# Optimization experiments

Measured on AMD Instinct MI355X. Metric: run time of the kernel, lower is better.

Reference implementation:

```python
import jax, jax.numpy as jnp
import numpy as np
from jax import lax

B, T, I, H, L, C = 256, 512, 128, 256, 2, 10


def _lstm_layer(x_tm, lengths, W_ih, W_hh, b_ih, b_hh):
    # x_tm: [T, B, in]; lengths: [B]
    b = b_ih + b_hh  # [4H]
    h0 = jnp.zeros((x_tm.shape[1], H), x_tm.dtype)
    c0 = jnp.zeros_like(h0)

    def step(carry, inp):
        h, c = carry
        x_t, t = inp
        gates = x_t @ W_ih.T + h @ W_hh.T + b  # [B, 4H]
        i, f, g, o = jnp.split(gates, 4, axis=-1)
        i = jax.nn.sigmoid(i); f = jax.nn.sigmoid(f)
        g = jnp.tanh(g);        o = jax.nn.sigmoid(o)
        c_new = f * c + i * g
        h_new = o * jnp.tanh(c_new)
        m = (t < lengths)[:, None]  # freeze state past each sequence's length
        h = jnp.where(m, h_new, h)
        c = jnp.where(m, c_new, c)
        return (h, c), h

    (hT, cT), h_seq = lax.scan(step, (h0, c0), (x_tm, jnp.arange(x_tm.shape[0])))
    return h_seq, hT


def setup_inputs() -> dict:
    key = jax.random.key(0)
    ks = jax.random.split(key, 16)
    s_i = 1.0 / np.sqrt(H)
    inp = {
        'x': jax.random.normal(ks[0], (B, T, I), jnp.float32),
        'lengths': jax.random.randint(ks[1], (B,), 1, T + 1),
        'W_fc': jax.random.uniform(ks[2], (C, H), jnp.float32, -s_i, s_i),
        'b_fc': jax.random.uniform(ks[3], (C,), jnp.float32, -s_i, s_i),
    }
    for l in range(L):
        in_dim = I if l == 0 else H
        k0, k1, k2, k3 = jax.random.split(jax.random.fold_in(key, 100 + l), 4)
        inp[f'W_ih_{l}'] = jax.random.uniform(k0, (4 * H, in_dim), jnp.float32, -s_i, s_i)
        inp[f'W_hh_{l}'] = jax.random.uniform(k1, (4 * H, H), jnp.float32, -s_i, s_i)
        inp[f'b_ih_{l}'] = jax.random.uniform(k2, (4 * H,), jnp.float32, -s_i, s_i)
        inp[f'b_hh_{l}'] = jax.random.uniform(k3, (4 * H,), jnp.float32, -s_i, s_i)
    return inp


def reference(x, lengths, W_fc, b_fc,
              W_ih_0, W_hh_0, b_ih_0, b_hh_0,
              W_ih_1, W_hh_1, b_ih_1, b_hh_1):
    layer_params = [(W_ih_0, W_hh_0, b_ih_0, b_hh_0),
                    (W_ih_1, W_hh_1, b_ih_1, b_hh_1)]
    seq = jnp.swapaxes(x, 0, 1)  # [T, B, I] time-major
    hT = None
    for (W_ih, W_hh, b_ih, b_hh) in layer_params:
        seq, hT = _lstm_layer(seq, lengths, W_ih, W_hh, b_ih, b_hh)
    logits = hT @ W_fc.T + b_fc  # final hidden state of last layer
    return jax.nn.softmax(logits, axis=1)
```

## Files before the change

### kernel.cpp

```cpp
#include <hip/hip_runtime.h>

#define TT 512
#define BB 256
#define II 128
#define HH 256
#define CC 10

typedef __attribute__((ext_vector_type(8))) _Float16 f16x8;
typedef __attribute__((ext_vector_type(4))) _Float16 f16x4;
typedef __attribute__((ext_vector_type(4))) float    f32x4;

__device__ __forceinline__ float fsig(float x){ return 1.0f/(1.0f+__expf(-x)); }
__device__ __forceinline__ float ftanh(float x){ return 2.0f/(1.0f+__expf(-2.0f*x)) - 1.0f; }


template<bool FAST>
__device__ __forceinline__ unsigned cpoll(unsigned* p){
  unsigned v;
  if constexpr(FAST){
    unsigned z = 0u;
    asm volatile("global_atomic_add %0, %1, %2, off sc0\n\ts_waitcnt vmcnt(0)"
                 : "=v"(v) : "v"(p), "v"(z) : "memory");
  } else {
    v = __hip_atomic_fetch_add(p, 0u, __ATOMIC_RELAXED, __HIP_MEMORY_SCOPE_AGENT);
  }
  return v;
}
template<bool FAST>
__device__ __forceinline__ unsigned poll_until(unsigned* p, unsigned tgt){
  unsigned v = 0;
  if((threadIdx.x & 63) == 0){
    v = cpoll<FAST>(p);
    while(v < tgt){ __builtin_amdgcn_s_sleep(2); v = cpoll<FAST>(p); }
  }
  unsigned u = __builtin_amdgcn_readfirstlane(v);
  asm volatile("" ::: "memory");
  return u;
}
template<bool FAST>
__device__ __forceinline__ void arrive1(unsigned* p){
  if constexpr(FAST){
    unsigned one = 1u;
    asm volatile("global_atomic_add %0, %1, off" :: "v"(p), "v"(one) : "memory");
  } else {
    (void)__hip_atomic_fetch_add(p, 1u, __ATOMIC_RELAXED, __HIP_MEMORY_SCOPE_AGENT);
  }
}
template<bool FAST>
__device__ __forceinline__ void store_h16(_Float16* p, _Float16 vv){
  unsigned b32 = (unsigned)__builtin_bit_cast(unsigned short, vv);
  if constexpr(FAST)
    asm volatile("global_store_short %0, %1, off" :: "v"(p), "v"(b32) : "memory");
  else
    asm volatile("global_store_short %0, %1, off sc0 sc1" :: "v"(p), "v"(b32) : "memory");
}
template<bool FAST>
__device__ __forceinline__ f16x8 load_ring(const _Float16* p){
  f16x8 r;
  if constexpr(FAST)
    asm volatile("global_load_dwordx4 %0, %1, off sc0" : "=v"(r) : "v"(p) : "memory");
  else
    asm volatile("global_load_dwordx4 %0, %1, off sc0 sc1" : "=v"(r) : "v"(p) : "memory");
  return r;
}
#define PIN(x) asm volatile("" : "+v"(x))

template<int KXT, bool IS_L1, bool FAST>
__device__ __forceinline__ void run_wave(
    const _Float16* __restrict__ xin,
    const _Float16* __restrict__ Wh,
    const _Float16* __restrict__ Wx,
    const float* __restrict__ b_ih, const float* __restrict__ b_hh,
    const int* __restrict__ lengths,
    _Float16* __restrict__ hbuf,
    float* __restrict__ hT,
    unsigned* cown, unsigned* cprod, int gb, int gj)
{
  constexpr int KXV = KXT*32;
  const int lane = threadIdx.x & 63;
  const int quad = lane >> 4;
  const int l15  = lane & 15;
  const int koff = quad << 3;
  const int b0   = gb << 4;
  const int u    = (gj << 4) + l15;

  f16x8 wh[4][8], wx[4][KXT];
  float bias[4];
#pragma unroll
  for(int g=0; g<4; ++g){
    const int row = g*HH + u;
#pragma unroll
    for(int kt=0; kt<8; ++kt){
      wh[g][kt] = *(const f16x8*)(Wh + (size_t)row*HH + kt*32 + koff);
      PIN(wh[g][kt]);
    }
#pragma unroll
    for(int kt=0; kt<KXT; ++kt){
      wx[g][kt] = *(const f16x8*)(Wx + (size_t)row*KXV + kt*32 + koff);
      PIN(wx[g][kt]);
    }
    bias[g] = b_ih[row] + b_hh[row];
  }

  int sb[4], len[4]; float cs[4], hs[4];
#pragma unroll
  for(int r=0; r<4; ++r){
    sb[r]  = b0 + (quad<<2) + r;
    len[r] = lengths[sb[r]];
    cs[r] = 0.f; hs[r] = 0.f;
  }

  unsigned lastp = 0, lasto = 0;

  f16x8 axn[KXT];
  if(!IS_L1){
    const _Float16* xp = xin + ((size_t)(b0+l15)*TT + 0)*KXV + koff;
#pragma unroll
    for(int kt=0; kt<KXT; ++kt) axn[kt] = *(const f16x8*)(xp + kt*32);
  }

  for(int t=0; t<TT; ++t){
    f16x8 ax[KXT];
    if(IS_L1){
      const unsigned tgtp = 16u*(unsigned)(t+1);
      if(lastp < tgtp) lastp = poll_until<FAST>(cprod, tgtp);
      const _Float16* xp = xin + ((size_t)t*BB + b0 + l15)*HH + koff;
#pragma unroll
      for(int kt=0; kt<KXT; ++kt) ax[kt] = *(const f16x8*)(xp + kt*32);
    } else {
#pragma unroll
      for(int kt=0; kt<KXT; ++kt) ax[kt] = axn[kt];
    }

    if(t > 0){
      const unsigned tgto = 16u*(unsigned)t;
      if(lasto < tgto) lasto = poll_until<FAST>(cown, tgto);
    }
    f16x8 ah[8];
    if(t > 0){
      if(IS_L1){
        const _Float16* hp = hbuf + (((size_t)((t-1)&3))*BB + b0 + l15)*HH + koff;
#pragma unroll
        for(int kt=0; kt<8; ++kt) ah[kt] = load_ring<FAST>(hp + kt*32);
      } else {
        const _Float16* hp = hbuf + ((size_t)(t-1)*BB + b0 + l15)*HH + koff;
#pragma unroll
        for(int kt=0; kt<8; ++kt) ah[kt] = *(const f16x8*)(hp + kt*32);
      }
    }

    f32x4 acc[4];
#pragma unroll
    for(int g=0; g<4; ++g) acc[g] = (f32x4){bias[g],bias[g],bias[g],bias[g]};
#pragma unroll
    for(int kt=0; kt<KXT; ++kt)
#pragma unroll
      for(int g=0; g<4; ++g)
        acc[g] = __builtin_amdgcn_mfma_f32_16x16x32_f16(ax[kt], wx[g][kt], acc[g], 0,0,0);

    if(t > 0){
      if(IS_L1){
        asm volatile("s_waitcnt vmcnt(0)"
          : "+v"(ah[0]),"+v"(ah[1]),"+v"(ah[2]),"+v"(ah[3]),
            "+v"(ah[4]),"+v"(ah[5]),"+v"(ah[6]),"+v"(ah[7]) :: "memory");
      }
#pragma unroll
      for(int kt=0; kt<8; ++kt)
#pragma unroll
        for(int g=0; g<4; ++g)
          acc[g] = __builtin_amdgcn_mfma_f32_16x16x32_f16(ah[kt], wh[g][kt], acc[g], 0,0,0);
    }

#pragma unroll
    for(int r=0; r<4; ++r){
      float iv = fsig (acc[0][r]);
      float fv = fsig (acc[1][r]);
      float gv = ftanh(acc[2][r]);
      float ov = fsig (acc[3][r]);
      float cn = fv*cs[r] + iv*gv;
      float hn = ov*ftanh(cn);
      if(t < len[r]){ cs[r] = cn; hs[r] = hn; }
      _Float16* hp = IS_L1
        ? hbuf + (((size_t)(t&3))*BB + sb[r])*HH + u
        : hbuf + ((size_t)t*BB + sb[r])*HH + u;
      store_h16<FAST>(hp, (_Float16)hs[r]);
      if(IS_L1 && t == TT-1) hT[(size_t)sb[r]*HH + u] = hs[r];
    }

    asm volatile("s_waitcnt vmcnt(0)" ::: "memory");
    if(lane == 0) arrive1<FAST>(cown);

    if(!IS_L1 && t+1 < TT){
      const _Float16* xp = xin + ((size_t)(b0+l15)*TT + (t+1))*KXV + koff;
#pragma unroll
      for(int kt=0; kt<KXT; ++kt) axn[kt] = *(const f16x8*)(xp + kt*32);
    }
  }
}

__global__ __launch_bounds__(64, 1)
void lstm_fused(const _Float16* __restrict__ xc,
                const _Float16* __restrict__ Wh0, const _Float16* __restrict__ Wx0,
                const _Float16* __restrict__ Wh1, const _Float16* __restrict__ Wx1,
                const float* __restrict__ b_ih0, const float* __restrict__ b_hh0,
                const float* __restrict__ b_ih1, const float* __restrict__ b_hh1,
                const int* __restrict__ lens,
                _Float16* __restrict__ h0seq, _Float16* __restrict__ h1ring,
                float* __restrict__ hT, unsigned* __restrict__ ctr)
{
  const int blk   = blockIdx.x;
  const int layer = blk >> 8;
  const int gb    = blk & 15;
  const int gj    = (blk >> 4) & 15;
  const int lane  = threadIdx.x & 63;
  unsigned* c0    = ctr + gb*32;
  unsigned* c1    = ctr + (16+gb)*32;
  unsigned* xcds  = ctr + 1024;
  unsigned* cinit = ctr + 1536;

  unsigned myx;
  asm volatile("s_getreg_b32 %0, hwreg(HW_REG_XCC_ID)" : "=s"(myx));
  if(lane == 0){
    asm volatile("global_store_dword %0, %1, off sc0 sc1" :: "v"(xcds + blk), "v"(myx) : "memory");
    asm volatile("s_waitcnt vmcnt(0)" ::: "memory");
    (void)__hip_atomic_fetch_add(cinit, 1u, __ATOMIC_RELAXED, __HIP_MEMORY_SCOPE_AGENT);
  }
  unsigned iv = 0;
  if(lane == 0){
    iv = __hip_atomic_fetch_add(cinit, 0u, __ATOMIC_RELAXED, __HIP_MEMORY_SCOPE_AGENT);
    while(iv < 512u){ __builtin_amdgcn_s_sleep(8);
      iv = __hip_atomic_fetch_add(cinit, 0u, __ATOMIC_RELAXED, __HIP_MEMORY_SCOPE_AGENT); }
  }
  (void)__builtin_amdgcn_readfirstlane(iv);
  asm volatile("" ::: "memory");
  unsigned pv = myx;
  if(lane < 32){
    const unsigned* pp = xcds + ((lane < 16) ? (gb + 16*lane)
                                             : (256 + gb + 16*(lane-16)));
    asm volatile("global_load_dword %0, %1, off sc0 sc1\n\ts_waitcnt vmcnt(0)"
                 : "=v"(pv) : "v"(pp) : "memory");
  }
  const bool fast = (__ballot(pv == myx) == ~0ull);

  if(layer == 0){
    if(fast) run_wave<4,false,true >(xc, Wh0, Wx0, b_ih0, b_hh0, lens, h0seq,
                                     nullptr, c0, nullptr, gb, gj);
    else     run_wave<4,false,false>(xc, Wh0, Wx0, b_ih0, b_hh0, lens, h0seq,
                                     nullptr, c0, nullptr, gb, gj);
  } else {
    if(fast) run_wave<8,true ,true >(h0seq, Wh1, Wx1, b_ih1, b_hh1, lens, h1ring,
                                     hT, c1, c0, gb, gj);
    else     run_wave<8,true ,false>(h0seq, Wh1, Wx1, b_ih1, b_hh1, lens, h1ring,
                                     hT, c1, c0, gb, gj);
  }
}

__global__ __launch_bounds__(256)
void cvt4(const float* __restrict__ in, _Float16* __restrict__ out, int n4)
{
  int i = blockIdx.x*256 + threadIdx.x;
  if(i < n4){
    float4 v = ((const float4*)in)[i];
    f16x4 o;
    o[0]=(_Float16)v.x; o[1]=(_Float16)v.y; o[2]=(_Float16)v.z; o[3]=(_Float16)v.w;
    ((f16x4*)out)[i] = o;
  }
}

__global__ __launch_bounds__(64)
void fc_softmax(const float* __restrict__ hT,
                const float* __restrict__ W_fc,
                const float* __restrict__ b_fc,
                float* __restrict__ out)
{
  const int b = blockIdx.x;
  const int lane = threadIdx.x;
  float p[CC];
#pragma unroll
  for (int c = 0; c < CC; ++c) p[c] = 0.f;
  const float* hb = hT + b * HH;
  for (int k = lane; k < HH; k += 64){
    float hv = hb[k];
#pragma unroll
    for (int c = 0; c < CC; ++c) p[c] += hv * W_fc[c * HH + k];
  }
#pragma unroll
  for (int c = 0; c < CC; ++c){
#pragma unroll
    for (int off = 32; off > 0; off >>= 1) p[c] += __shfl_down(p[c], off);
  }
  if (lane == 0){
    float m = -1e30f;
#pragma unroll
    for (int c = 0; c < CC; ++c){ p[c] += b_fc[c]; m = fmaxf(m, p[c]); }
    float ssum = 0.f;
#pragma unroll
    for (int c = 0; c < CC; ++c){ p[c] = __expf(p[c] - m); ssum += p[c]; }
    float inv = 1.0f / ssum;
#pragma unroll
    for (int c = 0; c < CC; ++c) out[b * CC + c] = p[c] * inv;
  }
}

extern "C" void kernel_launch(void* const* d_in, const int* in_sizes, int n_in,
                              void* d_out, int out_size, void* d_ws, size_t ws_size,
                              hipStream_t stream) {
  const float* x      = (const float*)d_in[0];
  const int*   lens   = (const int*)  d_in[1];
  const float* W_fc   = (const float*)d_in[2];
  const float* b_fc   = (const float*)d_in[3];
  const float* W_ih0  = (const float*)d_in[4];
  const float* W_hh0  = (const float*)d_in[5];
  const float* b_ih0  = (const float*)d_in[6];
  const float* b_hh0  = (const float*)d_in[7];
  const float* W_ih1  = (const float*)d_in[8];
  const float* W_hh1  = (const float*)d_in[9];
  const float* b_ih1  = (const float*)d_in[10];
  const float* b_hh1  = (const float*)d_in[11];
  float* out = (float*)d_out;

  char* ws = (char*)d_ws;
  unsigned* ctr  = (unsigned*)ws;
  float*    hT   = (float*)(ws + 8192);
  _Float16* Wh0c = (_Float16*)(ws + 270336);
  _Float16* Wx0c = (_Float16*)(ws + 794624);
  _Float16* Wh1c = (_Float16*)(ws + 1056768);
  _Float16* Wx1c = (_Float16*)(ws + 1581056);
  _Float16* xc   = (_Float16*)(ws + 2105344);
  _Float16* h0   = (_Float16*)(ws + 35659776);
  _Float16* h1r  = (_Float16*)(ws + 102768640);

  hipMemsetAsync(ws, 0, 8192, stream);

  cvt4<<<dim3((BB*TT*II/4 + 255)/256), dim3(256), 0, stream>>>(x,     xc,   BB*TT*II/4);
  cvt4<<<dim3((4*HH*HH/4  + 255)/256), dim3(256), 0, stream>>>(W_hh0, Wh0c, 4*HH*HH/4);
  cvt4<<<dim3((4*HH*II/4  + 255)/256), dim3(256), 0, stream>>>(W_ih0, Wx0c, 4*HH*II/4);
  cvt4<<<dim3((4*HH*HH/4  + 255)/256), dim3(256), 0, stream>>>(W_hh1, Wh1c, 4*HH*HH/4);
  cvt4<<<dim3((4*HH*HH/4  + 255)/256), dim3(256), 0, stream>>>(W_ih1, Wx1c, 4*HH*HH/4);

  lstm_fused<<<dim3(512), dim3(64), 0, stream>>>(
      xc, Wh0c, Wx0c, Wh1c, Wx1c, b_ih0, b_hh0, b_ih1, b_hh1, lens,
      h0, h1r, hT, ctr);

  fc_softmax<<<dim3(BB), dim3(64), 0, stream>>>(hT, W_fc, b_fc, out);
}
```

Measured before the change: 1.476 ms.

## Interleave two batch groups per wave to hide recurrent sync latency

Each persistent wave now handles two independent batch groups (set and set+8) instead of one, halving the grid to 256 blocks. While one group computes, the wave samples the other group's counters non-blockingly and prefetches its h and x operands, so the cross-block barrier and load latency of one group overlap the MFMA and elementwise work of the other. This trades per-wave serial work (twice the math per step) for fewer idle waits, and adds a more complex speculative-prefetch path with fallback polling.

Result: slower. 2.866 ms (+94.1%).

```diff
diff --git a/kernel.cpp b/kernel.cpp
--- a/kernel.cpp
+++ b/kernel.cpp
@@ -15,35 +15,48 @@
 
 
 template<bool FAST>
-__device__ __forceinline__ unsigned cpoll(unsigned* p){
-  unsigned v;
-  if constexpr(FAST){
-    unsigned z = 0u;
-    asm volatile("global_atomic_add %0, %1, %2, off sc0\n\ts_waitcnt vmcnt(0)"
-                 : "=v"(v) : "v"(p), "v"(z) : "memory");
-  } else {
-    v = __hip_atomic_fetch_add(p, 0u, __ATOMIC_RELAXED, __HIP_MEMORY_SCOPE_AGENT);
-  }
-  return v;
-}
-template<bool FAST>
-__device__ __forceinline__ unsigned poll_until(unsigned* p, unsigned tgt){
+__device__ __forceinline__ unsigned poll_rmw(unsigned* p, unsigned tgt){
   unsigned v = 0;
   if((threadIdx.x & 63) == 0){
-    v = cpoll<FAST>(p);
-    while(v < tgt){ __builtin_amdgcn_s_sleep(2); v = cpoll<FAST>(p); }
+    if constexpr(FAST){
+      unsigned z = 0u;
+      asm volatile("global_atomic_add %0, %1, %2, off sc0\n\ts_waitcnt vmcnt(0)"
+                   : "=v"(v) : "v"(p), "v"(z) : "memory");
+      while(v < tgt){
+        __builtin_amdgcn_s_sleep(2);
+        asm volatile("global_atomic_add %0, %1, %2, off sc0\n\ts_waitcnt vmcnt(0)"
+                     : "=v"(v) : "v"(p), "v"(z) : "memory");
+      }
+    } else {
+      v = __hip_atomic_fetch_add(p, 0u, __ATOMIC_RELAXED, __HIP_MEMORY_SCOPE_AGENT);
+      while(v < tgt){ __builtin_amdgcn_s_sleep(2);
+        v = __hip_atomic_fetch_add(p, 0u, __ATOMIC_RELAXED, __HIP_MEMORY_SCOPE_AGENT); }
+    }
   }
   unsigned u = __builtin_amdgcn_readfirstlane(v);
   asm volatile("" ::: "memory");
   return u;
 }
 template<bool FAST>
+__device__ __forceinline__ unsigned sample_rmw(unsigned* p){
+  if constexpr(FAST){
+    unsigned v, z = 0u;
+    asm volatile("global_atomic_add %0, %1, %2, off sc0"
+                 : "=v"(v) : "v"(p), "v"(z) : "memory");
+    return v;
+  } else {
+    return __hip_atomic_fetch_add(p, 0u, __ATOMIC_RELAXED, __HIP_MEMORY_SCOPE_AGENT);
+  }
+}
+template<bool FAST>
 __device__ __forceinline__ void arrive1(unsigned* p){
-  if constexpr(FAST){
-    unsigned one = 1u;
-    asm volatile("global_atomic_add %0, %1, off" :: "v"(p), "v"(one) : "memory");
-  } else {
-    (void)__hip_atomic_fetch_add(p, 1u, __ATOMIC_RELAXED, __HIP_MEMORY_SCOPE_AGENT);
+  if((threadIdx.x & 63) == 0){
+    if constexpr(FAST){
+      unsigned one = 1u;
+      asm volatile("global_atomic_add %0, %1, off" :: "v"(p), "v"(one) : "memory");
+    } else {
+      (void)__hip_atomic_fetch_add(p, 1u, __ATOMIC_RELAXED, __HIP_MEMORY_SCOPE_AGENT);
+    }
   }
 }
 template<bool FAST>
@@ -55,18 +68,37 @@
     asm volatile("global_store_short %0, %1, off sc0 sc1" :: "v"(p), "v"(b32) : "memory");
 }
 template<bool FAST>
-__device__ __forceinline__ f16x8 load_ring(const _Float16* p){
-  f16x8 r;
+__device__ __forceinline__ void ld16_ring(f16x8& r, const _Float16* p){
   if constexpr(FAST)
     asm volatile("global_load_dwordx4 %0, %1, off sc0" : "=v"(r) : "v"(p) : "memory");
   else
     asm volatile("global_load_dwordx4 %0, %1, off sc0 sc1" : "=v"(r) : "v"(p) : "memory");
-  return r;
+}
+__device__ __forceinline__ void ld16_pl(f16x8& r, const _Float16* p){
+  asm volatile("global_load_dwordx4 %0, %1, off" : "=v"(r) : "v"(p) : "memory");
 }
 #define PIN(x) asm volatile("" : "+v"(x))
+#define TIE4(A) "+v"(A[0]),"+v"(A[1]),"+v"(A[2]),"+v"(A[3])
+#define TIE8(A) TIE4(A),"+v"(A[4]),"+v"(A[5]),"+v"(A[6]),"+v"(A[7])
+
+template<bool FAST>
+__device__ __forceinline__ void ew_store(int t, f32x4 acc[4], float* cs, float* hs,
+    const int* len, _Float16* hbase, int sb0, int u){
+#pragma unroll
+  for(int r=0; r<4; ++r){
+    float iv = fsig (acc[0][r]);
+    float fv = fsig (acc[1][r]);
+    float gv = ftanh(acc[2][r]);
+    float ov = fsig (acc[3][r]);
+    float cn_ = fv*cs[r] + iv*gv;
+    float hn  = ov*ftanh(cn_);
+    if(t < len[r]){ cs[r] = cn_; hs[r] = hn; }
+    store_h16<FAST>(hbase + (size_t)(sb0+r)*HH + u, (_Float16)hs[r]);
+  }
+}
 
 template<int KXT, bool IS_L1, bool FAST>
-__device__ __forceinline__ void run_wave(
+__device__ __forceinline__ void run_wave2(
     const _Float16* __restrict__ xin,
     const _Float16* __restrict__ Wh,
     const _Float16* __restrict__ Wx,
@@ -74,14 +106,15 @@
     const int* __restrict__ lengths,
     _Float16* __restrict__ hbuf,
     float* __restrict__ hT,
-    unsigned* cown, unsigned* cprod, int gb, int gj)
+    unsigned* cownA, unsigned* cownB,
+    unsigned* cprodA, unsigned* cprodB,
+    int set, int gj)
 {
   constexpr int KXV = KXT*32;
   const int lane = threadIdx.x & 63;
   const int quad = lane >> 4;
   const int l15  = lane & 15;
   const int koff = quad << 3;
-  const int b0   = gb << 4;
   const int u    = (gj << 4) + l15;
 
   f16x8 wh[4][8], wx[4][KXT];
@@ -102,53 +135,54 @@
     bias[g] = b_ih[row] + b_hh[row];
   }
 
-  int sb[4], len[4]; float cs[4], hs[4];
-#pragma unroll
-  for(int r=0; r<4; ++r){
-    sb[r]  = b0 + (quad<<2) + r;
-    len[r] = lengths[sb[r]];
-    cs[r] = 0.f; hs[r] = 0.f;
-  }
-
-  unsigned lastp = 0, lasto = 0;
-
-  f16x8 axn[KXT];
-  if(!IS_L1){
-    const _Float16* xp = xin + ((size_t)(b0+l15)*TT + 0)*KXV + koff;
-#pragma unroll
-    for(int kt=0; kt<KXT; ++kt) axn[kt] = *(const f16x8*)(xp + kt*32);
-  }
-
-  for(int t=0; t<TT; ++t){
-    f16x8 ax[KXT];
-    if(IS_L1){
-      const unsigned tgtp = 16u*(unsigned)(t+1);
-      if(lastp < tgtp) lastp = poll_until<FAST>(cprod, tgtp);
-      const _Float16* xp = xin + ((size_t)t*BB + b0 + l15)*HH + koff;
-#pragma unroll
-      for(int kt=0; kt<KXT; ++kt) ax[kt] = *(const f16x8*)(xp + kt*32);
+  const int gb[2] = {set, set + 8};
+  unsigned* cown [2] = {cownA, cownB};
+  unsigned* cprod[2] = {cprodA, cprodB};
+  int len[2][4]; float cs[2][4], hs[2][4];
+#pragma unroll
+  for(int c=0; c<2; ++c){
+    const int sb0 = gb[c]*16 + quad*4;
+#pragma unroll
+    for(int r=0; r<4; ++r){
+      len[c][r] = lengths[sb0+r];
+      cs[c][r] = 0.f; hs[c][r] = 0.f;
+    }
+  }
+
+  f16x8 ah[8], ax[KXT];
+  unsigned sampO[2] = {0,0}, sampP[2] = {0,0};
+  bool pfok[2] = {false,false};
+
+  auto LOADAH = [&](int gbase, int t){
+    if constexpr(IS_L1){
+      const _Float16* hp = hbuf + (((size_t)((t-1)&3))*BB + gbase + l15)*HH + koff;
+#pragma unroll
+      for(int kt=0; kt<8; ++kt) ld16_ring<FAST>(ah[kt], hp + kt*32);
     } else {
-#pragma unroll
-      for(int kt=0; kt<KXT; ++kt) ax[kt] = axn[kt];
-    }
-
-    if(t > 0){
-      const unsigned tgto = 16u*(unsigned)t;
-      if(lasto < tgto) lasto = poll_until<FAST>(cown, tgto);
-    }
-    f16x8 ah[8];
-    if(t > 0){
-      if(IS_L1){
-        const _Float16* hp = hbuf + (((size_t)((t-1)&3))*BB + b0 + l15)*HH + koff;
-#pragma unroll
-        for(int kt=0; kt<8; ++kt) ah[kt] = load_ring<FAST>(hp + kt*32);
-      } else {
-        const _Float16* hp = hbuf + ((size_t)(t-1)*BB + b0 + l15)*HH + koff;
-#pragma unroll
-        for(int kt=0; kt<8; ++kt) ah[kt] = *(const f16x8*)(hp + kt*32);
-      }
-    }
-
+      const _Float16* hp = hbuf + ((size_t)(t-1)*BB + gbase + l15)*HH + koff;
+#pragma unroll
+      for(int kt=0; kt<8; ++kt) ld16_pl(ah[kt], hp + kt*32);
+    }
+  };
+  auto LOADAX = [&](int gbase, int t){
+    if constexpr(IS_L1){
+      const _Float16* xp = xin + ((size_t)t*BB + gbase + l15)*HH + koff;
+#pragma unroll
+      for(int kt=0; kt<KXT; ++kt) ld16_pl(ax[kt], xp + kt*32);
+    } else {
+      const _Float16* xp = xin + ((size_t)(gbase + l15)*TT + t)*KXV + koff;
+#pragma unroll
+      for(int kt=0; kt<KXT; ++kt) ld16_pl(ax[kt], xp + kt*32);
+    }
+  };
+
+#pragma unroll
+  for(int c=0; c<2; ++c){
+    if constexpr(IS_L1) poll_rmw<FAST>(cprod[c], 16u);
+    LOADAX(gb[c]*16, 0);
+    if constexpr(KXT==8) asm volatile("s_waitcnt vmcnt(0)" : TIE8(ax) :: "memory");
+    else                 asm volatile("s_waitcnt vmcnt(0)" : TIE4(ax) :: "memory");
+    __builtin_amdgcn_sched_barrier(0);
     f32x4 acc[4];
 #pragma unroll
     for(int g=0; g<4; ++g) acc[g] = (f32x4){bias[g],bias[g],bias[g],bias[g]};
@@ -157,43 +191,85 @@
 #pragma unroll
       for(int g=0; g<4; ++g)
         acc[g] = __builtin_amdgcn_mfma_f32_16x16x32_f16(ax[kt], wx[g][kt], acc[g], 0,0,0);
-
-    if(t > 0){
-      if(IS_L1){
-        asm volatile("s_waitcnt vmcnt(0)"
-          : "+v"(ah[0]),"+v"(ah[1]),"+v"(ah[2]),"+v"(ah[3]),
-            "+v"(ah[4]),"+v"(ah[5]),"+v"(ah[6]),"+v"(ah[7]) :: "memory");
+    ew_store<FAST>(0, acc, cs[c], hs[c], len[c], hbuf, gb[c]*16 + quad*4, u);
+    asm volatile("s_waitcnt vmcnt(0)" ::: "memory");
+    arrive1<FAST>(cown[c]);
+  }
+  poll_rmw<FAST>(cown[0], 16u);
+  if constexpr(IS_L1) poll_rmw<FAST>(cprod[0], 32u);
+  LOADAH(gb[0]*16, 1); LOADAX(gb[0]*16, 1);
+  pfok[0] = true;
+  if(lane == 0){
+    sampO[1] = sample_rmw<FAST>(cown[1]);
+    if constexpr(IS_L1) sampP[1] = sample_rmw<FAST>(cprod[1]);
+  }
+
+#pragma unroll 1
+  for(int t=1; t<TT; ++t){
+#pragma unroll
+    for(int c=0; c<2; ++c){
+      const int cn = 1-c;
+      const int tn = (c==0) ? t : t+1;
+
+      if(!pfok[c]){
+        poll_rmw<FAST>(cown[c], 16u*(unsigned)t);
+        if constexpr(IS_L1) poll_rmw<FAST>(cprod[c], 16u*(unsigned)(t+1));
+        LOADAH(gb[c]*16, t); LOADAX(gb[c]*16, t);
       }
+      if constexpr(KXT==8) asm volatile("s_waitcnt vmcnt(0)" : TIE8(ah), TIE8(ax) :: "memory");
+      else                 asm volatile("s_waitcnt vmcnt(0)" : TIE8(ah), TIE4(ax) :: "memory");
+      __builtin_amdgcn_sched_barrier(0);
+
+      f32x4 acc[4];
+#pragma unroll
+      for(int g=0; g<4; ++g) acc[g] = (f32x4){bias[g],bias[g],bias[g],bias[g]};
+#pragma unroll
+      for(int kt=0; kt<KXT; ++kt)
+#pragma unroll
+        for(int g=0; g<4; ++g)
+          acc[g] = __builtin_amdgcn_mfma_f32_16x16x32_f16(ax[kt], wx[g][kt], acc[g], 0,0,0);
 #pragma unroll
       for(int kt=0; kt<8; ++kt)
 #pragma unroll
         for(int g=0; g<4; ++g)
           acc[g] = __builtin_amdgcn_mfma_f32_16x16x32_f16(ah[kt], wh[g][kt], acc[g], 0,0,0);
-    }
-
-#pragma unroll
-    for(int r=0; r<4; ++r){
-      float iv = fsig (acc[0][r]);
-      float fv = fsig (acc[1][r]);
-      float gv = ftanh(acc[2][r]);
-      float ov = fsig (acc[3][r]);
-      float cn = fv*cs[r] + iv*gv;
-      float hn = ov*ftanh(cn);
-      if(t < len[r]){ cs[r] = cn; hs[r] = hn; }
-      _Float16* hp = IS_L1
-        ? hbuf + (((size_t)(t&3))*BB + sb[r])*HH + u
-        : hbuf + ((size_t)t*BB + sb[r])*HH + u;
-      store_h16<FAST>(hp, (_Float16)hs[r]);
-      if(IS_L1 && t == TT-1) hT[(size_t)sb[r]*HH + u] = hs[r];
-    }
-
-    asm volatile("s_waitcnt vmcnt(0)" ::: "memory");
-    if(lane == 0) arrive1<FAST>(cown);
-
-    if(!IS_L1 && t+1 < TT){
-      const _Float16* xp = xin + ((size_t)(b0+l15)*TT + (t+1))*KXV + koff;
-#pragma unroll
-      for(int kt=0; kt<KXT; ++kt) axn[kt] = *(const f16x8*)(xp + kt*32);
+      __builtin_amdgcn_sched_barrier(0);
+
+      if(tn < TT){
+        asm volatile("s_waitcnt vmcnt(0)"
+                     : "+v"(sampO[cn]), "+v"(sampP[cn]) :: "memory");
+        __builtin_amdgcn_sched_barrier(0);
+        unsigned so = __builtin_amdgcn_readfirstlane(sampO[cn]);
+        bool ok = (so >= 16u*(unsigned)tn);
+        if constexpr(IS_L1){
+          unsigned sp = __builtin_amdgcn_readfirstlane(sampP[cn]);
+          ok = ok && (sp >= 16u*(unsigned)(tn+1));
+        }
+        pfok[cn] = ok;
+        if(ok){ LOADAH(gb[cn]*16, tn); LOADAX(gb[cn]*16, tn); }
+      }
+
+      {
+        _Float16* hbase = IS_L1 ? hbuf + (size_t)(t&3)*BB*HH
+                                : hbuf + (size_t)t*BB*HH;
+        const int sb0 = gb[c]*16 + quad*4;
+        ew_store<FAST>(t, acc, cs[c], hs[c], len[c], hbase, sb0, u);
+        if constexpr(IS_L1){
+          if(t == TT-1){
+#pragma unroll
+            for(int r=0; r<4; ++r) hT[(size_t)(sb0+r)*HH + u] = hs[c][r];
+          }
+        }
+      }
+
+      asm volatile("s_waitcnt vmcnt(0)" ::: "memory");
+      arrive1<FAST>(cown[c]);
+      if(t+1 < TT){
+        if(lane == 0){
+          sampO[c] = sample_rmw<FAST>(cown[c]);
+          if constexpr(IS_L1) sampP[c] = sample_rmw<FAST>(cprod[c]);
+        }
+      }
     }
   }
 }
@@ -208,13 +284,16 @@
                 _Float16* __restrict__ h0seq, _Float16* __restrict__ h1ring,
                 float* __restrict__ hT, unsigned* __restrict__ ctr)
 {
-  const int blk   = blockIdx.x;
-  const int layer = blk >> 8;
-  const int gb    = blk & 15;
-  const int gj    = (blk >> 4) & 15;
-  const int lane  = threadIdx.x & 63;
-  unsigned* c0    = ctr + gb*32;
-  unsigned* c1    = ctr + (16+gb)*32;
+  const int blk  = blockIdx.x;
+  const bool L1k = blk >= 128;
+  const int  i   = L1k ? blk - 128 : blk;
+  const int  set = i & 7;
+  const int  gj  = i >> 3;
+  const int lane = threadIdx.x & 63;
+  unsigned* c0a = ctr + set*32;
+  unsigned* c0b = ctr + (set+8)*32;
+  unsigned* c1a = ctr + (16+set)*32;
+  unsigned* c1b = ctr + (16+set+8)*32;
   unsigned* xcds  = ctr + 1024;
   unsigned* cinit = ctr + 1536;
 
@@ -228,30 +307,30 @@
   unsigned iv = 0;
   if(lane == 0){
     iv = __hip_atomic_fetch_add(cinit, 0u, __ATOMIC_RELAXED, __HIP_MEMORY_SCOPE_AGENT);
-    while(iv < 512u){ __builtin_amdgcn_s_sleep(8);
+    while(iv < 256u){ __builtin_amdgcn_s_sleep(8);
       iv = __hip_atomic_fetch_add(cinit, 0u, __ATOMIC_RELAXED, __HIP_MEMORY_SCOPE_AGENT); }
   }
   (void)__builtin_amdgcn_readfirstlane(iv);
   asm volatile("" ::: "memory");
   unsigned pv = myx;
   if(lane < 32){
-    const unsigned* pp = xcds + ((lane < 16) ? (gb + 16*lane)
-                                             : (256 + gb + 16*(lane-16)));
+    const unsigned* pp = xcds + ((lane < 16) ? (set + 8*lane)
+                                             : (128 + set + 8*(lane-16)));
     asm volatile("global_load_dword %0, %1, off sc0 sc1\n\ts_waitcnt vmcnt(0)"
                  : "=v"(pv) : "v"(pp) : "memory");
   }
   const bool fast = (__ballot(pv == myx) == ~0ull);
 
-  if(layer == 0){
-    if(fast) run_wave<4,false,true >(xc, Wh0, Wx0, b_ih0, b_hh0, lens, h0seq,
-                                     nullptr, c0, nullptr, gb, gj);
-    else     run_wave<4,false,false>(xc, Wh0, Wx0, b_ih0, b_hh0, lens, h0seq,
-                                     nullptr, c0, nullptr, gb, gj);
+  if(!L1k){
+    if(fast) run_wave2<4,false,true >(xc, Wh0, Wx0, b_ih0, b_hh0, lens, h0seq,
+                                      nullptr, c0a, c0b, nullptr, nullptr, set, gj);
+    else     run_wave2<4,false,false>(xc, Wh0, Wx0, b_ih0, b_hh0, lens, h0seq,
+                                      nullptr, c0a, c0b, nullptr, nullptr, set, gj);
   } else {
-    if(fast) run_wave<8,true ,true >(h0seq, Wh1, Wx1, b_ih1, b_hh1, lens, h1ring,
-                                     hT, c1, c0, gb, gj);
-    else     run_wave<8,true ,false>(h0seq, Wh1, Wx1, b_ih1, b_hh1, lens, h1ring,
-                                     hT, c1, c0, gb, gj);
+    if(fast) run_wave2<8,true ,true >(h0seq, Wh1, Wx1, b_ih1, b_hh1, lens, h1ring,
+                                      hT, c1a, c1b, c0a, c0b, set, gj);
+    else     run_wave2<8,true ,false>(h0seq, Wh1, Wx1, b_ih1, b_hh1, lens, h1ring,
+                                      hT, c1a, c1b, c0a, c0b, set, gj);
   }
 }
 
@@ -338,7 +417,7 @@
   cvt4<<<dim3((4*HH*HH/4  + 255)/256), dim3(256), 0, stream>>>(W_hh1, Wh1c, 4*HH*HH/4);
   cvt4<<<dim3((4*HH*HH/4  + 255)/256), dim3(256), 0, stream>>>(W_ih1, Wx1c, 4*HH*HH/4);
 
-  lstm_fused<<<dim3(512), dim3(64), 0, stream>>>(
+  lstm_fused<<<dim3(256), dim3(64), 0, stream>>>(
       xc, Wh0c, Wx0c, Wh1c, Wx1c, b_ih0, b_hh0, b_ih1, b_hh1, lens,
       h0, h1r, hT, ctr);
 
```
